# Kernel tuning notes

Measured on AMD Instinct MI355X. Metric: run time of the kernel, lower is better.

## Reference

```python
import jax, jax.numpy as jnp
import numpy as np

B, W, T, D = 64, 32, 4096, 128

def setup_inputs() -> dict:
    key = jax.random.key(0)
    ks = jax.random.split(key, 10)
    s = 1.0 / np.sqrt(D)
    return {
        "x": jax.random.normal(ks[0], (B, W, T), dtype=jnp.float32),
        "enc_w": jax.random.uniform(ks[1], (D, W), jnp.float32, -1/np.sqrt(W), 1/np.sqrt(W)),
        "enc_b": jax.random.uniform(ks[2], (D,), jnp.float32, -1/np.sqrt(W), 1/np.sqrt(W)),
        "w_ih": jax.random.uniform(ks[3], (3 * D, D), jnp.float32, -s, s),
        "w_hh": jax.random.uniform(ks[4], (3 * D, D), jnp.float32, -s, s),
        "b_ih": jax.random.uniform(ks[5], (3 * D,), jnp.float32, -s, s),
        "b_hh": jax.random.uniform(ks[6], (3 * D,), jnp.float32, -s, s),
        "dec_w": jax.random.uniform(ks[7], (1, D), jnp.float32, -s, s),
        "dec_b": jax.random.uniform(ks[8], (1,), jnp.float32, -s, s),
        "scale": jnp.ones((1,), dtype=jnp.float32),
        "noise_eps": jax.random.normal(ks[9], (B, T), dtype=jnp.float32),
    }

def reference(x, enc_w, enc_b, w_ih, w_hh, b_ih, b_hh, dec_w, dec_b, scale, noise_eps):
    # x: [B, W, T] -> src: [T, B, W]
    src = jnp.transpose(x, (2, 0, 1))
    encoded = src @ enc_w.T + enc_b  # [T, B, D] (dropout is identity at inference)

    def gru_step(h, xt):
        gi = xt @ w_ih.T + b_ih  # [B, 3D]
        gh = h @ w_hh.T + b_hh   # [B, 3D]
        i_r, i_z, i_n = jnp.split(gi, 3, axis=-1)
        h_r, h_z, h_n = jnp.split(gh, 3, axis=-1)
        r = jax.nn.sigmoid(i_r + h_r)
        z = jax.nn.sigmoid(i_z + h_z)
        n = jnp.tanh(i_n + r * h_n)
        h_new = (1.0 - z) * n + z * h
        return h_new, h_new

    h0 = jnp.zeros_like(encoded[0])
    _, res = jax.lax.scan(gru_step, h0, encoded)  # res: [T, B, D]

    out = encoded + res
    out = (out @ dec_w.T + dec_b)[..., 0]  # [T, B]
    out = out.T                            # [B, T]
    noise = scale * noise_eps              # scale * randn_like(x[:, -1, :])
    return jax.nn.relu(out + noise)
```

## Files before the change

kernel.cpp:

```cpp
#include <hip/hip_runtime.h>

#define NB 64
#define NW 32
#define NT 4096
#define ND 128

#define GI_STRIDE 388
#define HR_STRIDE 144

typedef __attribute__((ext_vector_type(8))) short short8;
typedef __attribute__((ext_vector_type(4))) float f32x4;

#define BAR_LGKM() asm volatile("s_waitcnt lgkmcnt(0)\n\ts_barrier" ::: "memory")

static __device__ __forceinline__ float sigm_f(float v) {
    float e = __builtin_amdgcn_exp2f(v * -1.4426950408889634f);
    return __builtin_amdgcn_rcpf(1.0f + e);
}
static __device__ __forceinline__ float tanh_f(float v) {
    float e = __builtin_amdgcn_exp2f(v * 2.8853900817779268f);
    return 1.0f - 2.0f * __builtin_amdgcn_rcpf(1.0f + e);
}
static __device__ __forceinline__ unsigned short f2bf(float f) {
    unsigned u = __float_as_uint(f);
    u += 0x7FFFu + ((u >> 16) & 1u);
    return (unsigned short)(u >> 16);
}

__global__ __launch_bounds__(256) void k_xv(
    const float* __restrict__ x, const float* __restrict__ enc_w,
    const float* __restrict__ enc_b, const float* __restrict__ dec_w,
    const float* __restrict__ dec_b, const float* __restrict__ scale,
    const float* __restrict__ noise, float* __restrict__ out)
{
    __shared__ float v_s[NW];
    __shared__ float c2_s;
    const int tid = threadIdx.x;
    if (tid < NW) {
        float s = 0.0f;
        for (int d = 0; d < ND; ++d) s = fmaf(enc_w[d * NW + tid], dec_w[d], s);
        v_s[tid] = s;
    } else if (tid == 64) {
        float s = 0.0f;
        for (int d = 0; d < ND; ++d) s = fmaf(enc_b[d], dec_w[d], s);
        c2_s = s + dec_b[0];
    }
    __syncthreads();
    const int flat = blockIdx.x * 256 + tid;
    const int b = flat >> 12;
    const int t = flat & (NT - 1);
    float acc = c2_s + scale[0] * noise[flat];
    const float* xr = x + (size_t)b * NW * NT + t;
    #pragma unroll
    for (int w = 0; w < NW; ++w) acc = fmaf(xr[(size_t)w * NT], v_s[w], acc);
    out[flat] = acc;
}

__global__ __launch_bounds__(512, 2) void k_gru(
    const float* __restrict__ x, const float* __restrict__ enc_w,
    const float* __restrict__ enc_b, const float* __restrict__ w_ih,
    const float* __restrict__ w_hh, const float* __restrict__ b_ih,
    const float* __restrict__ b_hh, const float* __restrict__ dec_w,
    float* out)
{
    __shared__ alignas(16) float gi_lds[64 * GI_STRIDE];
    __shared__ float encb_s[ND];
    __shared__ alignas(16) unsigned short h_ring[32 * HR_STRIDE];
    __shared__ alignas(16) float xv_lds[NT];
    __shared__ alignas(16) float out_lds[NT];

    const int tid  = threadIdx.x;
    const int b    = blockIdx.x;
    const int wv   = tid >> 6;
    const int lane = tid & 63;
    const int g    = lane >> 4;
    const int c    = lane & 15;
    const int d    = wv * 16 + c;

    const size_t xbase = (size_t)b * NW * NT;
    float* outb = out + (size_t)b * NT;
    float* encw_s = gi_lds;

    for (int i = tid; i < ND * NW; i += 512) encw_s[i] = enc_w[i];
    if (tid < ND) encb_s[tid] = enc_b[tid];
    for (int i = tid; i < 32 * HR_STRIDE; i += 512) h_ring[i] = 0;
    for (int i = tid; i < NT / 4; i += 512)
        ((float4*)xv_lds)[i] = ((const float4*)outb)[i];
    __syncthreads();

    short8 BR[4], BZ[4], BN[4];
    #pragma unroll
    for (int kt = 0; kt < 4; ++kt) {
        const float* pr = w_hh + (size_t)(0*ND + d) * ND + kt*32 + g*8;
        const float* pz = w_hh + (size_t)(1*ND + d) * ND + kt*32 + g*8;
        const float* pn = w_hh + (size_t)(2*ND + d) * ND + kt*32 + g*8;
        #pragma unroll
        for (int i = 0; i < 8; ++i) {
            BR[kt][i] = (short)f2bf(pr[i]);
            BZ[kt][i] = (short)f2bf(pz[i]);
            BN[kt][i] = (short)f2bf(pn[i]);
        }
    }

    short8 BD[4];
    #pragma unroll
    for (int kt = 0; kt < 4; ++kt)
        #pragma unroll
        for (int i = 0; i < 8; ++i)
            BD[kt][i] = (short)f2bf(dec_w[kt*32 + g*8 + i]);

    short8 XR, XZ, XN;
    {
        const float* rr = w_ih + (size_t)(0*ND + d) * ND;
        const float* rz = w_ih + (size_t)(1*ND + d) * ND;
        const float* rn = w_ih + (size_t)(2*ND + d) * ND;
        #pragma unroll
        for (int i = 0; i < 8; ++i) {
            int w = g*8 + i;
            float ar = 0.0f, az = 0.0f, an = 0.0f;
            for (int dp = 0; dp < ND; ++dp) {
                float ew = encw_s[dp*NW + w];
                ar = fmaf(ew, rr[dp], ar);
                az = fmaf(ew, rz[dp], az);
                an = fmaf(ew, rn[dp], an);
            }
            XR[i] = (short)f2bf(ar); XZ[i] = (short)f2bf(az); XN[i] = (short)f2bf(an);
        }
    }

    float cR, cZ, cGN, cIN;
    {
        const float* rr = w_ih + (size_t)(0*ND + d) * ND;
        const float* rz = w_ih + (size_t)(1*ND + d) * ND;
        const float* rn = w_ih + (size_t)(2*ND + d) * ND;
        float b0 = b_ih[d], b1 = b_ih[ND+d], b2 = b_ih[2*ND+d];
        for (int dp = 0; dp < ND; ++dp) {
            float eb = encb_s[dp];
            b0 = fmaf(eb, rr[dp], b0);
            b1 = fmaf(eb, rz[dp], b1);
            b2 = fmaf(eb, rn[dp], b2);
        }
        cR  = b0 + b_hh[d];
        cZ  = b1 + b_hh[ND+d];
        cGN = b_hh[2*ND+d];
        cIN = b2;
    }
    const f32x4 cRv  = {cR, cR, cR, cR};
    const f32x4 cZv  = {cZ, cZ, cZ, cZ};
    const f32x4 cGNv = {cGN, cGN, cGN, cGN};
    const f32x4 cINv = {cIN, cIN, cIN, cIN};
    const f32x4 zv   = {0.f, 0.f, 0.f, 0.f};

    __syncthreads();

    float xf[16];
    #pragma unroll
    for (int q = 0; q < 16; ++q)
        xf[q] = x[xbase + (size_t)(g*8 + (q & 7)) * NT + ((q >> 3) * 16 + c)];
    {
        short8 xA0, xA1;
        #pragma unroll
        for (int i = 0; i < 8; ++i) { xA0[i] = (short)f2bf(xf[i]); xA1[i] = (short)f2bf(xf[8+i]); }
        f32x4 gR0 = __builtin_amdgcn_mfma_f32_16x16x32_bf16(xA0, XR, cRv, 0, 0, 0);
        f32x4 gR1 = __builtin_amdgcn_mfma_f32_16x16x32_bf16(xA1, XR, cRv, 0, 0, 0);
        f32x4 gZ0 = __builtin_amdgcn_mfma_f32_16x16x32_bf16(xA0, XZ, cZv, 0, 0, 0);
        f32x4 gZ1 = __builtin_amdgcn_mfma_f32_16x16x32_bf16(xA1, XZ, cZv, 0, 0, 0);
        f32x4 gN0 = __builtin_amdgcn_mfma_f32_16x16x32_bf16(xA0, XN, cINv, 0, 0, 0);
        f32x4 gN1 = __builtin_amdgcn_mfma_f32_16x16x32_bf16(xA1, XN, cINv, 0, 0, 0);
        #pragma unroll
        for (int r = 0; r < 4; ++r) {
            int ti = 4*g + r;
            gi_lds[(ti     )*GI_STRIDE +       d] = gR0[r];
            gi_lds[(ti     )*GI_STRIDE + 128 + d] = gZ0[r];
            gi_lds[(ti     )*GI_STRIDE + 256 + d] = gN0[r];
            gi_lds[(ti + 16)*GI_STRIDE +       d] = gR1[r];
            gi_lds[(ti + 16)*GI_STRIDE + 128 + d] = gZ1[r];
            gi_lds[(ti + 16)*GI_STRIDE + 256 + d] = gN1[r];
        }
    }
    #pragma unroll
    for (int q = 0; q < 16; ++q)
        xf[q] = x[xbase + (size_t)(g*8 + (q & 7)) * NT + (32 + (q >> 3) * 16 + c)];

    __syncthreads();

    float h = 0.0f;

    #pragma unroll 1
    for (int t = 0; t < NT; ++t) {
        const short8* hp = (const short8*)(h_ring + (size_t)((t + 31) & 31) * HR_STRIDE);
        const short8 HA0 = hp[0*4 + g];
        const short8 HA1 = hp[1*4 + g];
        const short8 HA2 = hp[2*4 + g];
        const short8 HA3 = hp[3*4 + g];

        const float* gp = gi_lds + (size_t)(t & 63) * GI_STRIDE + d;
        const float giR = gp[0];
        const float giZ = gp[128];
        const float giN = gp[256];

        f32x4 aR1 = __builtin_amdgcn_mfma_f32_16x16x32_bf16(HA0, BR[0], zv,  0, 0, 0);
        f32x4 aR2 = __builtin_amdgcn_mfma_f32_16x16x32_bf16(HA2, BR[2], zv,  0, 0, 0);
        aR1 = __builtin_amdgcn_mfma_f32_16x16x32_bf16(HA1, BR[1], aR1, 0, 0, 0);
        aR2 = __builtin_amdgcn_mfma_f32_16x16x32_bf16(HA3, BR[3], aR2, 0, 0, 0);
        f32x4 aZ1 = __builtin_amdgcn_mfma_f32_16x16x32_bf16(HA0, BZ[0], zv,  0, 0, 0);
        f32x4 aZ2 = __builtin_amdgcn_mfma_f32_16x16x32_bf16(HA2, BZ[2], zv,  0, 0, 0);
        aZ1 = __builtin_amdgcn_mfma_f32_16x16x32_bf16(HA1, BZ[1], aZ1, 0, 0, 0);
        aZ2 = __builtin_amdgcn_mfma_f32_16x16x32_bf16(HA3, BZ[3], aZ2, 0, 0, 0);
        f32x4 aN1 = __builtin_amdgcn_mfma_f32_16x16x32_bf16(HA0, BN[0], cGNv, 0, 0, 0);
        f32x4 aN2 = __builtin_amdgcn_mfma_f32_16x16x32_bf16(HA2, BN[2], zv,  0, 0, 0);
        aN1 = __builtin_amdgcn_mfma_f32_16x16x32_bf16(HA1, BN[1], aN1, 0, 0, 0);
        aN2 = __builtin_amdgcn_mfma_f32_16x16x32_bf16(HA3, BN[3], aN2, 0, 0, 0);

        if ((t & 31) == 8) {
            const int t0n = (t & ~31) + 32;
            if (t0n < NT) {
                short8 xA0, xA1;
                #pragma unroll
                for (int i = 0; i < 8; ++i) { xA0[i] = (short)f2bf(xf[i]); xA1[i] = (short)f2bf(xf[8+i]); }
                f32x4 gR0 = __builtin_amdgcn_mfma_f32_16x16x32_bf16(xA0, XR, cRv, 0, 0, 0);
                f32x4 gR1 = __builtin_amdgcn_mfma_f32_16x16x32_bf16(xA1, XR, cRv, 0, 0, 0);
                f32x4 gZ0 = __builtin_amdgcn_mfma_f32_16x16x32_bf16(xA0, XZ, cZv, 0, 0, 0);
                f32x4 gZ1 = __builtin_amdgcn_mfma_f32_16x16x32_bf16(xA1, XZ, cZv, 0, 0, 0);
                f32x4 gN0 = __builtin_amdgcn_mfma_f32_16x16x32_bf16(xA0, XN, cINv, 0, 0, 0);
                f32x4 gN1 = __builtin_amdgcn_mfma_f32_16x16x32_bf16(xA1, XN, cINv, 0, 0, 0);
                const int rbw = t0n & 63;
                #pragma unroll
                for (int r = 0; r < 4; ++r) {
                    int ti = rbw + 4*g + r;
                    gi_lds[(ti     )*GI_STRIDE +       d] = gR0[r];
                    gi_lds[(ti     )*GI_STRIDE + 128 + d] = gZ0[r];
                    gi_lds[(ti     )*GI_STRIDE + 256 + d] = gN0[r];
                    gi_lds[(ti + 16)*GI_STRIDE +       d] = gR1[r];
                    gi_lds[(ti + 16)*GI_STRIDE + 128 + d] = gZ1[r];
                    gi_lds[(ti + 16)*GI_STRIDE + 256 + d] = gN1[r];
                }
                const int t0p = t0n + 32;
                if (t0p < NT) {
                    #pragma unroll
                    for (int q = 0; q < 16; ++q)
                        xf[q] = x[xbase + (size_t)(g*8 + (q & 7)) * NT + (t0p + (q >> 3) * 16 + c)];
                }
            }
        }

        if ((t & 15) == 0 && t >= 16 && wv == (((t >> 4) - 1) & 7)) {
            const short8* hq = (const short8*)(h_ring + (size_t)(((t - 16) & 31) + c) * HR_STRIDE);
            short8 AD0 = hq[0*4 + g];
            short8 AD1 = hq[1*4 + g];
            short8 AD2 = hq[2*4 + g];
            short8 AD3 = hq[3*4 + g];
            f32x4 aD1 = __builtin_amdgcn_mfma_f32_16x16x32_bf16(AD0, BD[0], zv, 0, 0, 0);
            f32x4 aD2 = __builtin_amdgcn_mfma_f32_16x16x32_bf16(AD2, BD[2], zv, 0, 0, 0);
            aD1 = __builtin_amdgcn_mfma_f32_16x16x32_bf16(AD1, BD[1], aD1, 0, 0, 0);
            aD2 = __builtin_amdgcn_mfma_f32_16x16x32_bf16(AD3, BD[3], aD2, 0, 0, 0);
            if (c == 0) {
                #pragma unroll
                for (int r = 0; r < 4; ++r)
                    out_lds[(t - 16) + 4*g + r] = aD1[r] + aD2[r];
            }
        }

        float R  = aR1[0] + aR2[0] + giR;
        float r_ = sigm_f(R);
        float Z  = aZ1[0] + aZ2[0] + giZ;
        float z_ = sigm_f(Z);
        float GN = aN1[0] + aN2[0];
        float n_ = tanh_f(fmaf(r_, GN, giN));
        h = fmaf(z_, h - n_, n_);
        if (lane < 16) h_ring[(size_t)(t & 31) * HR_STRIDE + d] = f2bf(h);
        BAR_LGKM();
    }

    if (wv == 7) {
        const short8* hq = (const short8*)(h_ring + (size_t)(16 + c) * HR_STRIDE);
        short8 AD0 = hq[0*4 + g];
        short8 AD1 = hq[1*4 + g];
        short8 AD2 = hq[2*4 + g];
        short8 AD3 = hq[3*4 + g];
        f32x4 aD1 = __builtin_amdgcn_mfma_f32_16x16x32_bf16(AD0, BD[0], zv, 0, 0, 0);
        f32x4 aD2 = __builtin_amdgcn_mfma_f32_16x16x32_bf16(AD2, BD[2], zv, 0, 0, 0);
        aD1 = __builtin_amdgcn_mfma_f32_16x16x32_bf16(AD1, BD[1], aD1, 0, 0, 0);
        aD2 = __builtin_amdgcn_mfma_f32_16x16x32_bf16(AD3, BD[3], aD2, 0, 0, 0);
        if (c == 0) {
            #pragma unroll
            for (int r = 0; r < 4; ++r)
                out_lds[(NT - 16) + 4*g + r] = aD1[r] + aD2[r];
        }
    }
    __syncthreads();
    for (int i = tid; i < NT / 4; i += 512) {
        float4 o = ((const float4*)out_lds)[i];
        float4 v = ((const float4*)xv_lds)[i];
        float4 r;
        r.x = fmaxf(o.x + v.x, 0.0f);
        r.y = fmaxf(o.y + v.y, 0.0f);
        r.z = fmaxf(o.z + v.z, 0.0f);
        r.w = fmaxf(o.w + v.w, 0.0f);
        ((float4*)outb)[i] = r;
    }
}

extern "C" void kernel_launch(void* const* d_in, const int* in_sizes, int n_in,
                              void* d_out, int out_size, void* d_ws, size_t ws_size,
                              hipStream_t stream) {
    const float* x      = (const float*)d_in[0];
    const float* enc_w  = (const float*)d_in[1];
    const float* enc_b  = (const float*)d_in[2];
    const float* w_ih   = (const float*)d_in[3];
    const float* w_hh   = (const float*)d_in[4];
    const float* b_ih   = (const float*)d_in[5];
    const float* b_hh   = (const float*)d_in[6];
    const float* dec_w  = (const float*)d_in[7];
    const float* dec_b  = (const float*)d_in[8];
    const float* scale  = (const float*)d_in[9];
    const float* noise  = (const float*)d_in[10];
    float* out = (float*)d_out;

    k_xv<<<(NB * NT) / 256, 256, 0, stream>>>(x, enc_w, enc_b, dec_w, dec_b, scale, noise, out);
    k_gru<<<NB, 512, 0, stream>>>(x, enc_w, enc_b, w_ih, w_hh, b_ih, b_hh, dec_w, out);
}
```

Baseline: 1.801 ms.

## Halve GRU block to 4 waves, each computing 32 hidden units

Shrinks the GRU block from 8 to 4 wavefronts, so each wave handles 32 hidden columns with two sets of MFMA weight fragments. The input-gate precompute now runs every 16 steps instead of 32. The gate values are stored interleaved per column so one vector LDS load fetches all three. The intent is to make the per-step barrier cheaper with fewer waves and to raise MFMA ILP per wave. The cost is doubled per-wave MFMA work and register pressure on the serial critical path.

```diff
diff --git a/kernel.cpp b/kernel.cpp
--- a/kernel.cpp
+++ b/kernel.cpp
@@ -5,7 +5,7 @@
 #define NT 4096
 #define ND 128
 
-#define GI_STRIDE 388
+#define GI_DW 516
 #define HR_STRIDE 144
 
 typedef __attribute__((ext_vector_type(8))) short short8;
@@ -56,14 +56,14 @@
     out[flat] = acc;
 }
 
-__global__ __launch_bounds__(512, 2) void k_gru(
+__global__ __launch_bounds__(256, 1) void k_gru(
     const float* __restrict__ x, const float* __restrict__ enc_w,
     const float* __restrict__ enc_b, const float* __restrict__ w_ih,
     const float* __restrict__ w_hh, const float* __restrict__ b_ih,
     const float* __restrict__ b_hh, const float* __restrict__ dec_w,
     float* out)
 {
-    __shared__ alignas(16) float gi_lds[64 * GI_STRIDE];
+    __shared__ alignas(16) float gi_lds[32 * GI_DW];
     __shared__ float encb_s[ND];
     __shared__ alignas(16) unsigned short h_ring[32 * HR_STRIDE];
     __shared__ alignas(16) float xv_lds[NT];
@@ -75,30 +75,39 @@
     const int lane = tid & 63;
     const int g    = lane >> 4;
     const int c    = lane & 15;
-    const int d    = wv * 16 + c;
+    const int hi   = g & 1;
+    const int d0   = wv * 32 + c;
+    const int d1   = d0 + 16;
+    const int dl   = wv * 32 + (lane & 31);
 
     const size_t xbase = (size_t)b * NW * NT;
     float* outb = out + (size_t)b * NT;
     float* encw_s = gi_lds;
 
-    for (int i = tid; i < ND * NW; i += 512) encw_s[i] = enc_w[i];
+    for (int i = tid; i < ND * NW; i += 256) encw_s[i] = enc_w[i];
     if (tid < ND) encb_s[tid] = enc_b[tid];
-    for (int i = tid; i < 32 * HR_STRIDE; i += 512) h_ring[i] = 0;
-    for (int i = tid; i < NT / 4; i += 512)
+    for (int i = tid; i < 32 * HR_STRIDE; i += 256) h_ring[i] = 0;
+    for (int i = tid; i < NT / 4; i += 256)
         ((float4*)xv_lds)[i] = ((const float4*)outb)[i];
     __syncthreads();
 
-    short8 BR[4], BZ[4], BN[4];
+    short8 BR0[4], BZ0[4], BN0[4], BR1[4], BZ1[4], BN1[4];
     #pragma unroll
     for (int kt = 0; kt < 4; ++kt) {
-        const float* pr = w_hh + (size_t)(0*ND + d) * ND + kt*32 + g*8;
-        const float* pz = w_hh + (size_t)(1*ND + d) * ND + kt*32 + g*8;
-        const float* pn = w_hh + (size_t)(2*ND + d) * ND + kt*32 + g*8;
+        const float* pr0 = w_hh + (size_t)(0*ND + d0) * ND + kt*32 + g*8;
+        const float* pz0 = w_hh + (size_t)(1*ND + d0) * ND + kt*32 + g*8;
+        const float* pn0 = w_hh + (size_t)(2*ND + d0) * ND + kt*32 + g*8;
+        const float* pr1 = w_hh + (size_t)(0*ND + d1) * ND + kt*32 + g*8;
+        const float* pz1 = w_hh + (size_t)(1*ND + d1) * ND + kt*32 + g*8;
+        const float* pn1 = w_hh + (size_t)(2*ND + d1) * ND + kt*32 + g*8;
         #pragma unroll
         for (int i = 0; i < 8; ++i) {
-            BR[kt][i] = (short)f2bf(pr[i]);
-            BZ[kt][i] = (short)f2bf(pz[i]);
-            BN[kt][i] = (short)f2bf(pn[i]);
+            BR0[kt][i] = (short)f2bf(pr0[i]);
+            BZ0[kt][i] = (short)f2bf(pz0[i]);
+            BN0[kt][i] = (short)f2bf(pn0[i]);
+            BR1[kt][i] = (short)f2bf(pr1[i]);
+            BZ1[kt][i] = (short)f2bf(pz1[i]);
+            BN1[kt][i] = (short)f2bf(pn1[i]);
         }
     }
 
@@ -109,78 +118,98 @@
         for (int i = 0; i < 8; ++i)
             BD[kt][i] = (short)f2bf(dec_w[kt*32 + g*8 + i]);
 
-    short8 XR, XZ, XN;
+    short8 XR0, XZ0, XN0, XR1, XZ1, XN1;
     {
-        const float* rr = w_ih + (size_t)(0*ND + d) * ND;
-        const float* rz = w_ih + (size_t)(1*ND + d) * ND;
-        const float* rn = w_ih + (size_t)(2*ND + d) * ND;
+        const float* rr0 = w_ih + (size_t)(0*ND + d0) * ND;
+        const float* rz0 = w_ih + (size_t)(1*ND + d0) * ND;
+        const float* rn0 = w_ih + (size_t)(2*ND + d0) * ND;
+        const float* rr1 = w_ih + (size_t)(0*ND + d1) * ND;
+        const float* rz1 = w_ih + (size_t)(1*ND + d1) * ND;
+        const float* rn1 = w_ih + (size_t)(2*ND + d1) * ND;
         #pragma unroll
         for (int i = 0; i < 8; ++i) {
             int w = g*8 + i;
-            float ar = 0.0f, az = 0.0f, an = 0.0f;
+            float ar0 = 0.f, az0 = 0.f, an0 = 0.f, ar1 = 0.f, az1 = 0.f, an1 = 0.f;
             for (int dp = 0; dp < ND; ++dp) {
                 float ew = encw_s[dp*NW + w];
-                ar = fmaf(ew, rr[dp], ar);
-                az = fmaf(ew, rz[dp], az);
-                an = fmaf(ew, rn[dp], an);
+                ar0 = fmaf(ew, rr0[dp], ar0);
+                az0 = fmaf(ew, rz0[dp], az0);
+                an0 = fmaf(ew, rn0[dp], an0);
+                ar1 = fmaf(ew, rr1[dp], ar1);
+                az1 = fmaf(ew, rz1[dp], az1);
+                an1 = fmaf(ew, rn1[dp], an1);
             }
-            XR[i] = (short)f2bf(ar); XZ[i] = (short)f2bf(az); XN[i] = (short)f2bf(an);
-        }
-    }
-
-    float cR, cZ, cGN, cIN;
+            XR0[i] = (short)f2bf(ar0); XZ0[i] = (short)f2bf(az0); XN0[i] = (short)f2bf(an0);
+            XR1[i] = (short)f2bf(ar1); XZ1[i] = (short)f2bf(az1); XN1[i] = (short)f2bf(an1);
+        }
+    }
+
+    float cR0, cZ0, cGN0, cIN0, cR1, cZ1, cGN1, cIN1;
     {
-        const float* rr = w_ih + (size_t)(0*ND + d) * ND;
-        const float* rz = w_ih + (size_t)(1*ND + d) * ND;
-        const float* rn = w_ih + (size_t)(2*ND + d) * ND;
-        float b0 = b_ih[d], b1 = b_ih[ND+d], b2 = b_ih[2*ND+d];
+        const float* rr0 = w_ih + (size_t)(0*ND + d0) * ND;
+        const float* rz0 = w_ih + (size_t)(1*ND + d0) * ND;
+        const float* rn0 = w_ih + (size_t)(2*ND + d0) * ND;
+        const float* rr1 = w_ih + (size_t)(0*ND + d1) * ND;
+        const float* rz1 = w_ih + (size_t)(1*ND + d1) * ND;
+        const float* rn1 = w_ih + (size_t)(2*ND + d1) * ND;
+        float a0 = b_ih[d0], a1 = b_ih[ND+d0], a2 = b_ih[2*ND+d0];
+        float e0 = b_ih[d1], e1 = b_ih[ND+d1], e2 = b_ih[2*ND+d1];
         for (int dp = 0; dp < ND; ++dp) {
             float eb = encb_s[dp];
-            b0 = fmaf(eb, rr[dp], b0);
-            b1 = fmaf(eb, rz[dp], b1);
-            b2 = fmaf(eb, rn[dp], b2);
-        }
-        cR  = b0 + b_hh[d];
-        cZ  = b1 + b_hh[ND+d];
-        cGN = b_hh[2*ND+d];
-        cIN = b2;
-    }
-    const f32x4 cRv  = {cR, cR, cR, cR};
-    const f32x4 cZv  = {cZ, cZ, cZ, cZ};
-    const f32x4 cGNv = {cGN, cGN, cGN, cGN};
-    const f32x4 cINv = {cIN, cIN, cIN, cIN};
-    const f32x4 zv   = {0.f, 0.f, 0.f, 0.f};
-
-    __syncthreads();
-
-    float xf[16];
-    #pragma unroll
-    for (int q = 0; q < 16; ++q)
-        xf[q] = x[xbase + (size_t)(g*8 + (q & 7)) * NT + ((q >> 3) * 16 + c)];
+            a0 = fmaf(eb, rr0[dp], a0);
+            a1 = fmaf(eb, rz0[dp], a1);
+            a2 = fmaf(eb, rn0[dp], a2);
+            e0 = fmaf(eb, rr1[dp], e0);
+            e1 = fmaf(eb, rz1[dp], e1);
+            e2 = fmaf(eb, rn1[dp], e2);
+        }
+        cR0  = a0 + b_hh[d0];
+        cZ0  = a1 + b_hh[ND+d0];
+        cGN0 = b_hh[2*ND+d0];
+        cIN0 = a2;
+        cR1  = e0 + b_hh[d1];
+        cZ1  = e1 + b_hh[ND+d1];
+        cGN1 = b_hh[2*ND+d1];
+        cIN1 = e2;
+    }
+    const f32x4 cRv0  = {cR0, cR0, cR0, cR0};
+    const f32x4 cZv0  = {cZ0, cZ0, cZ0, cZ0};
+    const f32x4 cGNv0 = {cGN0, cGN0, cGN0, cGN0};
+    const f32x4 cINv0 = {cIN0, cIN0, cIN0, cIN0};
+    const f32x4 cRv1  = {cR1, cR1, cR1, cR1};
+    const f32x4 cZv1  = {cZ1, cZ1, cZ1, cZ1};
+    const f32x4 cGNv1 = {cGN1, cGN1, cGN1, cGN1};
+    const f32x4 cINv1 = {cIN1, cIN1, cIN1, cIN1};
+    const f32x4 zv    = {0.f, 0.f, 0.f, 0.f};
+
+    __syncthreads();
+
+    float xf[8];
+    #pragma unroll
+    for (int q = 0; q < 8; ++q)
+        xf[q] = x[xbase + (size_t)(g*8 + q) * NT + c];
     {
-        short8 xA0, xA1;
-        #pragma unroll
-        for (int i = 0; i < 8; ++i) { xA0[i] = (short)f2bf(xf[i]); xA1[i] = (short)f2bf(xf[8+i]); }
-        f32x4 gR0 = __builtin_amdgcn_mfma_f32_16x16x32_bf16(xA0, XR, cRv, 0, 0, 0);
-        f32x4 gR1 = __builtin_amdgcn_mfma_f32_16x16x32_bf16(xA1, XR, cRv, 0, 0, 0);
-        f32x4 gZ0 = __builtin_amdgcn_mfma_f32_16x16x32_bf16(xA0, XZ, cZv, 0, 0, 0);
-        f32x4 gZ1 = __builtin_amdgcn_mfma_f32_16x16x32_bf16(xA1, XZ, cZv, 0, 0, 0);
-        f32x4 gN0 = __builtin_amdgcn_mfma_f32_16x16x32_bf16(xA0, XN, cINv, 0, 0, 0);
-        f32x4 gN1 = __builtin_amdgcn_mfma_f32_16x16x32_bf16(xA1, XN, cINv, 0, 0, 0);
+        short8 xA;
+        #pragma unroll
+        for (int i = 0; i < 8; ++i) xA[i] = (short)f2bf(xf[i]);
+        f32x4 gR0 = __builtin_amdgcn_mfma_f32_16x16x32_bf16(xA, XR0, cRv0, 0, 0, 0);
+        f32x4 gZ0 = __builtin_amdgcn_mfma_f32_16x16x32_bf16(xA, XZ0, cZv0, 0, 0, 0);
+        f32x4 gN0 = __builtin_amdgcn_mfma_f32_16x16x32_bf16(xA, XN0, cINv0, 0, 0, 0);
+        f32x4 gR1 = __builtin_amdgcn_mfma_f32_16x16x32_bf16(xA, XR1, cRv1, 0, 0, 0);
+        f32x4 gZ1 = __builtin_amdgcn_mfma_f32_16x16x32_bf16(xA, XZ1, cZv1, 0, 0, 0);
+        f32x4 gN1 = __builtin_amdgcn_mfma_f32_16x16x32_bf16(xA, XN1, cINv1, 0, 0, 0);
         #pragma unroll
         for (int r = 0; r < 4; ++r) {
             int ti = 4*g + r;
-            gi_lds[(ti     )*GI_STRIDE +       d] = gR0[r];
-            gi_lds[(ti     )*GI_STRIDE + 128 + d] = gZ0[r];
-            gi_lds[(ti     )*GI_STRIDE + 256 + d] = gN0[r];
-            gi_lds[(ti + 16)*GI_STRIDE +       d] = gR1[r];
-            gi_lds[(ti + 16)*GI_STRIDE + 128 + d] = gZ1[r];
-            gi_lds[(ti + 16)*GI_STRIDE + 256 + d] = gN1[r];
-        }
-    }
-    #pragma unroll
-    for (int q = 0; q < 16; ++q)
-        xf[q] = x[xbase + (size_t)(g*8 + (q & 7)) * NT + (32 + (q >> 3) * 16 + c)];
+            f32x4 p0 = {gR0[r], gZ0[r], gN0[r], 0.f};
+            f32x4 p1 = {gR1[r], gZ1[r], gN1[r], 0.f};
+            *(f32x4*)(gi_lds + (size_t)ti * GI_DW + d0 * 4) = p0;
+            *(f32x4*)(gi_lds + (size_t)ti * GI_DW + d1 * 4) = p1;
+        }
+    }
+    #pragma unroll
+    for (int q = 0; q < 8; ++q)
+        xf[q] = x[xbase + (size_t)(g*8 + q) * NT + 16 + c];
 
     __syncthreads();
 
@@ -194,57 +223,73 @@
         const short8 HA2 = hp[2*4 + g];
         const short8 HA3 = hp[3*4 + g];
 
-        const float* gp = gi_lds + (size_t)(t & 63) * GI_STRIDE + d;
-        const float giR = gp[0];
-        const float giZ = gp[128];
-        const float giN = gp[256];
-
-        f32x4 aR1 = __builtin_amdgcn_mfma_f32_16x16x32_bf16(HA0, BR[0], zv,  0, 0, 0);
-        f32x4 aR2 = __builtin_amdgcn_mfma_f32_16x16x32_bf16(HA2, BR[2], zv,  0, 0, 0);
-        aR1 = __builtin_amdgcn_mfma_f32_16x16x32_bf16(HA1, BR[1], aR1, 0, 0, 0);
-        aR2 = __builtin_amdgcn_mfma_f32_16x16x32_bf16(HA3, BR[3], aR2, 0, 0, 0);
-        f32x4 aZ1 = __builtin_amdgcn_mfma_f32_16x16x32_bf16(HA0, BZ[0], zv,  0, 0, 0);
-        f32x4 aZ2 = __builtin_amdgcn_mfma_f32_16x16x32_bf16(HA2, BZ[2], zv,  0, 0, 0);
-        aZ1 = __builtin_amdgcn_mfma_f32_16x16x32_bf16(HA1, BZ[1], aZ1, 0, 0, 0);
-        aZ2 = __builtin_amdgcn_mfma_f32_16x16x32_bf16(HA3, BZ[3], aZ2, 0, 0, 0);
-        f32x4 aN1 = __builtin_amdgcn_mfma_f32_16x16x32_bf16(HA0, BN[0], cGNv, 0, 0, 0);
-        f32x4 aN2 = __builtin_amdgcn_mfma_f32_16x16x32_bf16(HA2, BN[2], zv,  0, 0, 0);
-        aN1 = __builtin_amdgcn_mfma_f32_16x16x32_bf16(HA1, BN[1], aN1, 0, 0, 0);
-        aN2 = __builtin_amdgcn_mfma_f32_16x16x32_bf16(HA3, BN[3], aN2, 0, 0, 0);
-
-        if ((t & 31) == 8) {
-            const int t0n = (t & ~31) + 32;
+        const f32x4 giv = *(const f32x4*)(gi_lds + (size_t)(t & 31) * GI_DW + dl * 4);
+
+        f32x4 aR1_0 = __builtin_amdgcn_mfma_f32_16x16x32_bf16(HA0, BR0[0], zv, 0, 0, 0);
+        f32x4 aR2_0 = __builtin_amdgcn_mfma_f32_16x16x32_bf16(HA2, BR0[2], zv, 0, 0, 0);
+        f32x4 aR1_1 = __builtin_amdgcn_mfma_f32_16x16x32_bf16(HA0, BR1[0], zv, 0, 0, 0);
+        f32x4 aR2_1 = __builtin_amdgcn_mfma_f32_16x16x32_bf16(HA2, BR1[2], zv, 0, 0, 0);
+        aR1_0 = __builtin_amdgcn_mfma_f32_16x16x32_bf16(HA1, BR0[1], aR1_0, 0, 0, 0);
+        aR2_0 = __builtin_amdgcn_mfma_f32_16x16x32_bf16(HA3, BR0[3], aR2_0, 0, 0, 0);
+        aR1_1 = __builtin_amdgcn_mfma_f32_16x16x32_bf16(HA1, BR1[1], aR1_1, 0, 0, 0);
+        aR2_1 = __builtin_amdgcn_mfma_f32_16x16x32_bf16(HA3, BR1[3], aR2_1, 0, 0, 0);
+        f32x4 aZ1_0 = __builtin_amdgcn_mfma_f32_16x16x32_bf16(HA0, BZ0[0], zv, 0, 0, 0);
+        f32x4 aZ2_0 = __builtin_amdgcn_mfma_f32_16x16x32_bf16(HA2, BZ0[2], zv, 0, 0, 0);
+        f32x4 aZ1_1 = __builtin_amdgcn_mfma_f32_16x16x32_bf16(HA0, BZ1[0], zv, 0, 0, 0);
+        f32x4 aZ2_1 = __builtin_amdgcn_mfma_f32_16x16x32_bf16(HA2, BZ1[2], zv, 0, 0, 0);
+        aZ1_0 = __builtin_amdgcn_mfma_f32_16x16x32_bf16(HA1, BZ0[1], aZ1_0, 0, 0, 0);
+        aZ2_0 = __builtin_amdgcn_mfma_f32_16x16x32_bf16(HA3, BZ0[3], aZ2_0, 0, 0, 0);
+        aZ1_1 = __builtin_amdgcn_mfma_f32_16x16x32_bf16(HA1, BZ1[1], aZ1_1, 0, 0, 0);
+        aZ2_1 = __builtin_amdgcn_mfma_f32_16x16x32_bf16(HA3, BZ1[3], aZ2_1, 0, 0, 0);
+        f32x4 aN1_0 = __builtin_amdgcn_mfma_f32_16x16x32_bf16(HA0, BN0[0], cGNv0, 0, 0, 0);
+        f32x4 aN2_0 = __builtin_amdgcn_mfma_f32_16x16x32_bf16(HA2, BN0[2], zv, 0, 0, 0);
+        f32x4 aN1_1 = __builtin_amdgcn_mfma_f32_16x16x32_bf16(HA0, BN1[0], cGNv1, 0, 0, 0);
+        f32x4 aN2_1 = __builtin_amdgcn_mfma_f32_16x16x32_bf16(HA2, BN1[2], zv, 0, 0, 0);
+        aN1_0 = __builtin_amdgcn_mfma_f32_16x16x32_bf16(HA1, BN0[1], aN1_0, 0, 0, 0);
+        aN2_0 = __builtin_amdgcn_mfma_f32_16x16x32_bf16(HA3, BN0[3], aN2_0, 0, 0, 0);
+        aN1_1 = __builtin_amdgcn_mfma_f32_16x16x32_bf16(HA1, BN1[1], aN1_1, 0, 0, 0);
+        aN2_1 = __builtin_amdgcn_mfma_f32_16x16x32_bf16(HA3, BN1[3], aN2_1, 0, 0, 0);
+
+        float R  = hi ? (aR1_1[0] + aR2_1[0]) : (aR1_0[0] + aR2_0[0]);
+        float Z  = hi ? (aZ1_1[0] + aZ2_1[0]) : (aZ1_0[0] + aZ2_0[0]);
+        float GN = hi ? (aN1_1[0] + aN2_1[0]) : (aN1_0[0] + aN2_0[0]);
+        float r_ = sigm_f(R + giv[0]);
+        float z_ = sigm_f(Z + giv[1]);
+        float n_ = tanh_f(fmaf(r_, GN, giv[2]));
+        h = fmaf(z_, h - n_, n_);
+        if (lane < 32) h_ring[(size_t)(t & 31) * HR_STRIDE + dl] = f2bf(h);
+
+        if ((t & 15) == 8) {
+            const int t0n = (t & ~15) + 16;
             if (t0n < NT) {
-                short8 xA0, xA1;
+                short8 xA;
                 #pragma unroll
-                for (int i = 0; i < 8; ++i) { xA0[i] = (short)f2bf(xf[i]); xA1[i] = (short)f2bf(xf[8+i]); }
-                f32x4 gR0 = __builtin_amdgcn_mfma_f32_16x16x32_bf16(xA0, XR, cRv, 0, 0, 0);
-                f32x4 gR1 = __builtin_amdgcn_mfma_f32_16x16x32_bf16(xA1, XR, cRv, 0, 0, 0);
-                f32x4 gZ0 = __builtin_amdgcn_mfma_f32_16x16x32_bf16(xA0, XZ, cZv, 0, 0, 0);
-                f32x4 gZ1 = __builtin_amdgcn_mfma_f32_16x16x32_bf16(xA1, XZ, cZv, 0, 0, 0);
-                f32x4 gN0 = __builtin_amdgcn_mfma_f32_16x16x32_bf16(xA0, XN, cINv, 0, 0, 0);
-                f32x4 gN1 = __builtin_amdgcn_mfma_f32_16x16x32_bf16(xA1, XN, cINv, 0, 0, 0);
-                const int rbw = t0n & 63;
+                for (int i = 0; i < 8; ++i) xA[i] = (short)f2bf(xf[i]);
+                f32x4 gR0 = __builtin_amdgcn_mfma_f32_16x16x32_bf16(xA, XR0, cRv0, 0, 0, 0);
+                f32x4 gZ0 = __builtin_amdgcn_mfma_f32_16x16x32_bf16(xA, XZ0, cZv0, 0, 0, 0);
+                f32x4 gN0 = __builtin_amdgcn_mfma_f32_16x16x32_bf16(xA, XN0, cINv0, 0, 0, 0);
+                f32x4 gR1 = __builtin_amdgcn_mfma_f32_16x16x32_bf16(xA, XR1, cRv1, 0, 0, 0);
+                f32x4 gZ1 = __builtin_amdgcn_mfma_f32_16x16x32_bf16(xA, XZ1, cZv1, 0, 0, 0);
+                f32x4 gN1 = __builtin_amdgcn_mfma_f32_16x16x32_bf16(xA, XN1, cINv1, 0, 0, 0);
+                const int rb = t0n & 31;
                 #pragma unroll
                 for (int r = 0; r < 4; ++r) {
-                    int ti = rbw + 4*g + r;
-                    gi_lds[(ti     )*GI_STRIDE +       d] = gR0[r];
-                    gi_lds[(ti     )*GI_STRIDE + 128 + d] = gZ0[r];
-                    gi_lds[(ti     )*GI_STRIDE + 256 + d] = gN0[r];
-                    gi_lds[(ti + 16)*GI_STRIDE +       d] = gR1[r];
-                    gi_lds[(ti + 16)*GI_STRIDE + 128 + d] = gZ1[r];
-                    gi_lds[(ti + 16)*GI_STRIDE + 256 + d] = gN1[r];
+                    int ti = rb + 4*g + r;
+                    f32x4 p0 = {gR0[r], gZ0[r], gN0[r], 0.f};
+                    f32x4 p1 = {gR1[r], gZ1[r], gN1[r], 0.f};
+                    *(f32x4*)(gi_lds + (size_t)ti * GI_DW + d0 * 4) = p0;
+                    *(f32x4*)(gi_lds + (size_t)ti * GI_DW + d1 * 4) = p1;
                 }
-                const int t0p = t0n + 32;
+                const int t0p = t0n + 16;
                 if (t0p < NT) {
                     #pragma unroll
-                    for (int q = 0; q < 16; ++q)
-                        xf[q] = x[xbase + (size_t)(g*8 + (q & 7)) * NT + (t0p + (q >> 3) * 16 + c)];
+                    for (int q = 0; q < 8; ++q)
+                        xf[q] = x[xbase + (size_t)(g*8 + q) * NT + t0p + c];
                 }
             }
         }
 
-        if ((t & 15) == 0 && t >= 16 && wv == (((t >> 4) - 1) & 7)) {
+        if ((t & 15) == 0 && t >= 16 && wv == (((t >> 4) - 1) & 3)) {
             const short8* hq = (const short8*)(h_ring + (size_t)(((t - 16) & 31) + c) * HR_STRIDE);
             short8 AD0 = hq[0*4 + g];
             short8 AD1 = hq[1*4 + g];
@@ -261,18 +306,10 @@
             }
         }
 
-        float R  = aR1[0] + aR2[0] + giR;
-        float r_ = sigm_f(R);
-        float Z  = aZ1[0] + aZ2[0] + giZ;
-        float z_ = sigm_f(Z);
-        float GN = aN1[0] + aN2[0];
-        float n_ = tanh_f(fmaf(r_, GN, giN));
-        h = fmaf(z_, h - n_, n_);
-        if (lane < 16) h_ring[(size_t)(t & 31) * HR_STRIDE + d] = f2bf(h);
         BAR_LGKM();
     }
 
-    if (wv == 7) {
+    if (wv == 0) {
         const short8* hq = (const short8*)(h_ring + (size_t)(16 + c) * HR_STRIDE);
         short8 AD0 = hq[0*4 + g];
         short8 AD1 = hq[1*4 + g];
@@ -289,7 +326,7 @@
         }
     }
     __syncthreads();
-    for (int i = tid; i < NT / 4; i += 512) {
+    for (int i = tid; i < NT / 4; i += 256) {
         float4 o = ((const float4*)out_lds)[i];
         float4 v = ((const float4*)xv_lds)[i];
         float4 r;
@@ -318,5 +355,5 @@
     float* out = (float*)d_out;
 
     k_xv<<<(NB * NT) / 256, 256, 0, stream>>>(x, enc_w, enc_b, dec_w, dec_b, scale, noise, out);
-    k_gru<<<NB, 512, 0, stream>>>(x, enc_w, enc_b, w_ih, w_hh, b_ih, b_hh, dec_w, out);
-}
+    k_gru<<<NB, 256, 0, stream>>>(x, enc_w, enc_b, w_ih, w_hh, b_ih, b_hh, dec_w, out);
+}
```

Measured after the change: 1.764 ms. 2.1% less time.
